# Performance work log

Measured on AMD Instinct MI355X. Metric: run time of the kernel, lower is better.

The kernel has to match this reference:

```python
import jax, jax.numpy as jnp
import numpy as np

B, L, D = 8, 4096, 384
DI, S, DTR, K = 768, 16, 24, 4  # d_inner, d_state, dt_rank, d_conv
NC = 40
EPS = 1e-5


def setup_inputs() -> dict:
    key = jax.random.key(0)
    ks = jax.random.split(key, 12)
    w = 0.02
    return {
        "x": jax.random.normal(ks[0], (B, L, D), jnp.float32),
        "ln_w": jnp.ones((D,), jnp.float32),
        "W_in": jax.random.normal(ks[1], (D, 2 * DI), jnp.float32) * w,
        "conv_w": jax.random.normal(ks[2], (DI, K), jnp.float32) * 0.1,
        "conv_b": jnp.zeros((DI,), jnp.float32),
        "W_xproj": jax.random.normal(ks[3], (DI, DTR + 2 * S), jnp.float32) * w,
        "W_dt": jax.random.normal(ks[4], (DTR, DI), jnp.float32) * 0.1,
        "dt_bias": jnp.full((DI,), -3.0, jnp.float32) + 0.1 * jax.random.normal(ks[5], (DI,), jnp.float32),
        "A_log": jnp.log(1.0 + jax.random.uniform(ks[6], (DI, S), jnp.float32) * 15.0),
        "Dskip": jnp.ones((DI,), jnp.float32),
        "W_out": jax.random.normal(ks[7], (DI, D), jnp.float32) * w,
        "W_fc": jax.random.normal(ks[8], (D, 256), jnp.float32) * w,
        "b_fc": jnp.zeros((256,), jnp.float32),
        "bn_gamma": jnp.ones((256,), jnp.float32),
        "bn_beta": jnp.zeros((256,), jnp.float32),
        "W_cls": jax.random.normal(ks[9], (256, NC), jnp.float32) * w,
        "b_cls": jnp.zeros((NC,), jnp.float32),
    }


def _silu(v):
    return v * jax.nn.sigmoid(v)


def _mamba_block(x, ln_w, W_in, conv_w, conv_b, W_xproj, W_dt, dt_bias, A_log, Dskip, W_out):
    # RMSNorm
    xn = x * jax.lax.rsqrt(jnp.mean(x * x, axis=-1, keepdims=True) + EPS) * ln_w
    xz = xn @ W_in                              # [B,L,2*DI]
    xp, z = jnp.split(xz, 2, axis=-1)
    # causal depthwise conv over sequence
    xp_t = jnp.transpose(xp, (0, 2, 1))         # [B,DI,L]
    xc = jax.lax.conv_general_dilated(
        xp_t, conv_w[:, None, :], window_strides=(1,), padding=[(K - 1, 0)],
        feature_group_count=DI, dimension_numbers=("NCH", "OIH", "NCH"))
    xc = _silu(xc + conv_b[None, :, None])
    xc = jnp.transpose(xc, (0, 2, 1))           # [B,L,DI]
    x_dbl = xc @ W_xproj                        # [B,L,DTR+2S]
    dt_r, Bm, Cm = jnp.split(x_dbl, [DTR, DTR + S], axis=-1)
    dt = jax.nn.softplus(dt_r @ W_dt + dt_bias)  # [B,L,DI]
    A = -jnp.exp(A_log)                          # [DI,S]

    def step(h, t):
        dt_t, B_t, C_t, x_t = t                  # [B,DI],[B,S],[B,S],[B,DI]
        dA = jnp.exp(dt_t[..., None] * A)        # [B,DI,S]
        h = dA * h + (dt_t * x_t)[..., None] * B_t[:, None, :]
        y = jnp.einsum("bds,bs->bd", h, C_t)
        return h, y

    tm = lambda a: jnp.transpose(a, (1, 0, 2))   # time-major
    h0 = jnp.zeros((x.shape[0], DI, S), x.dtype)
    _, ys = jax.lax.scan(step, h0, (tm(dt), tm(Bm), tm(Cm), tm(xc)))
    y = jnp.transpose(ys, (1, 0, 2)) + xc * Dskip  # [B,L,DI]
    y = y * _silu(z)
    return x + y @ W_out                          # residual


def reference(x, ln_w, W_in, conv_w, conv_b, W_xproj, W_dt, dt_bias, A_log,
              Dskip, W_out, W_fc, b_fc, bn_gamma, bn_beta, W_cls, b_cls):
    feats = _mamba_block(x, ln_w, W_in, conv_w, conv_b, W_xproj, W_dt, dt_bias,
                         A_log, Dskip, W_out)
    pooled = jnp.mean(feats, axis=1)             # global pool -> [B,D]
    h = pooled @ W_fc + b_fc                     # Fc
    mu = jnp.mean(h, axis=0)                     # Bn (batch stats)
    var = jnp.var(h, axis=0)
    h = (h - mu) * jax.lax.rsqrt(var + EPS) * bn_gamma + bn_beta
    h = jax.nn.relu(h)                           # Relu (dropout=eval no-op)
    return h @ W_cls + b_cls                     # logits [B,NC]
```

## Files before the change

### kernel.cpp

```cpp
#include <hip/hip_runtime.h>

typedef unsigned short ushort_t;
typedef unsigned int u32;
typedef float f32x4 __attribute__((ext_vector_type(4)));
typedef float f32x2 __attribute__((ext_vector_type(2)));
typedef __bf16 bf16x8 __attribute__((ext_vector_type(8)));

#define B_ 8
#define L_ 4096
#define D_ 384
#define DI_ 768
#define S_ 16
#define NC_ 40
#define ML_ (B_*L_)
#define NCHUNK 32
#define CL 128

constexpr size_t au(size_t x){ return (x + 255) & ~size_t(255); }
constexpr size_t O_FLAG = 0;
constexpr size_t O_LNW  = 256;
constexpr size_t O_CONVW= au(O_LNW  + 384*4);
constexpr size_t O_CONVB= au(O_CONVW+ 3072*4);
constexpr size_t O_WDT  = au(O_CONVB+ 768*4);
constexpr size_t O_DTB  = au(O_WDT  + 18432*4);
constexpr size_t O_A    = au(O_DTB  + 768*4);
constexpr size_t O_DSKIP= au(O_A    + 12288*4);
constexpr size_t O_WOUT = au(O_DSKIP+ 768*4);
constexpr size_t O_WFC  = au(O_WOUT + 294912*4);
constexpr size_t O_BFC  = au(O_WFC  + 98304*4);
constexpr size_t O_GAM  = au(O_BFC  + 256*4);
constexpr size_t O_BET  = au(O_GAM  + 256*4);
constexpr size_t O_WCLS = au(O_BET  + 256*4);
constexpr size_t O_BCLS = au(O_WCLS + 10240*4);
constexpr size_t O_XMEAN= au(O_BCLS + 40*4);
constexpr size_t O_YMEAN= au(O_XMEAN+ 3072*4);
constexpr size_t O_H    = au(O_YMEAN+ 6144*4);
constexpr size_t O_WINT = au(O_H    + 2048*4);
constexpr size_t O_WXT  = au(O_WINT + (size_t)589824*2);
constexpr size_t O_XP   = au(O_WXT  + (size_t)49152*2);
constexpr size_t O_XDBL = O_XP;
constexpr size_t O_FX   = au(O_XDBL + (size_t)ML_*56*4);
constexpr size_t FX_SZ  = (size_t)B_*NCHUNK*49*768*4;
constexpr size_t O_Z    = au(O_XP   + (size_t)ML_*768*2);
constexpr size_t O_XCU  = au(O_Z    + (size_t)ML_*768*2);
constexpr size_t O_XN   = O_XCU;
constexpr size_t O_XC   = O_XCU;
constexpr size_t WS_NEED= O_XCU + (size_t)ML_*768*2;
static_assert(O_FX + FX_SZ <= O_Z, "FX must fit in dead XP tail");

__device__ inline float bf2f(ushort_t u){ return __uint_as_float(((u32)u) << 16); }
__device__ inline ushort_t f2bf(float f){
    u32 x = __float_as_uint(f);
    u32 r = (x + 0x7fffu + ((x >> 16) & 1u)) >> 16;
    return (ushort_t)r;
}
__device__ inline float ldf(const void* p, long i, int flag){
    return flag ? bf2f(((const ushort_t*)p)[i]) : ((const float*)p)[i];
}
__device__ inline ushort_t ldbf(const void* p, long i, int flag){
    return flag ? ((const ushort_t*)p)[i] : f2bf(((const float*)p)[i]);
}
__device__ inline float sigm(float v){ return 1.f / (1.f + __expf(-v)); }

__device__ inline void gload_lds16(const void* g, void* l){
    __builtin_amdgcn_global_load_lds(
        (const __attribute__((address_space(1))) u32*)g,
        (__attribute__((address_space(3))) u32*)l, 16, 0, 0);
}

struct Ptrs { const void* p[17]; };

__global__ void k_detect(const void* x, char* ws){
    __shared__ float s[256];
    int tid = threadIdx.x;
    s[tid] = fabsf(bf2f(((const ushort_t*)x)[tid]));
    __syncthreads();
    for (int st = 128; st > 0; st >>= 1){
        if (tid < st) s[tid] = fmaxf(s[tid], s[tid + st]);
        __syncthreads();
    }
    if (tid == 0) *(int*)(ws + O_FLAG) = (s[0] < 1e4f) ? 1 : 0;
}

#define N_PREP 1082792L
__global__ __launch_bounds__(256) void k_prep(Ptrs ps, char* ws){
    const int flag = *(const int*)(ws + O_FLAG);
    long o = (long)blockIdx.x * 256 + threadIdx.x;
    if (o < 384){ ((float*)(ws+O_LNW))[o]  = ldf(ps.p[1],o,flag); return; }  o -= 384;
    if (o < 3072){ ((float*)(ws+O_CONVW))[o]= ldf(ps.p[3],o,flag); return; } o -= 3072;
    if (o < 768){ ((float*)(ws+O_CONVB))[o]= ldf(ps.p[4],o,flag); return; }  o -= 768;
    if (o < 18432){ ((float*)(ws+O_WDT))[o]= ldf(ps.p[6],o,flag); return; }  o -= 18432;
    if (o < 768){ ((float*)(ws+O_DTB))[o]  = ldf(ps.p[7],o,flag); return; }  o -= 768;
    if (o < 768){ ((float*)(ws+O_DSKIP))[o]= ldf(ps.p[9],o,flag); return; }  o -= 768;
    if (o < 294912){ ((float*)(ws+O_WOUT))[o]= ldf(ps.p[10],o,flag); return; } o -= 294912;
    if (o < 98304){ ((float*)(ws+O_WFC))[o]= ldf(ps.p[11],o,flag); return; } o -= 98304;
    if (o < 256){ ((float*)(ws+O_BFC))[o]  = ldf(ps.p[12],o,flag); return; } o -= 256;
    if (o < 256){ ((float*)(ws+O_GAM))[o]  = ldf(ps.p[13],o,flag); return; } o -= 256;
    if (o < 256){ ((float*)(ws+O_BET))[o]  = ldf(ps.p[14],o,flag); return; } o -= 256;
    if (o < 10240){ ((float*)(ws+O_WCLS))[o]= ldf(ps.p[15],o,flag); return; } o -= 10240;
    if (o < 40){ ((float*)(ws+O_BCLS))[o]  = ldf(ps.p[16],o,flag); return; } o -= 40;
    if (o < 12288){ ((float*)(ws+O_A))[o]  = -__expf(ldf(ps.p[8],o,flag)) * 1.4426950408889634f; return; } o -= 12288;
    if (o < 589824){
        long n = o / 384, k = o % 384;
        ((ushort_t*)(ws+O_WINT))[o] = ldbf(ps.p[2], k*1536 + n, flag); return;
    } o -= 589824;
    if (o < 49152){
        long n = o / 768, k = o % 768;
        ((ushort_t*)(ws+O_WXT))[o] = (n < 56) ? ldbf(ps.p[5], k*56 + n, flag) : (ushort_t)0;
        return;
    } o -= 49152;
    if (o < 3072){ ((float*)(ws+O_XMEAN))[o] = 0.f; return; }
}

__global__ __launch_bounds__(128) void k_rmsnorm(const void* x, char* ws){
    const int flag = *(const int*)(ws + O_FLAG);
    const float* lnw = (const float*)(ws + O_LNW);
    ushort_t* xn = (ushort_t*)(ws + O_XN);
    long row = blockIdx.x;
    int tid = threadIdx.x;
    float v[3];
    if (flag){
        const ushort_t* xb = (const ushort_t*)x;
        #pragma unroll
        for (int c = 0; c < 3; c++) v[c] = bf2f(xb[row*384 + tid + c*128]);
    } else {
        const float* xf = (const float*)x;
        #pragma unroll
        for (int c = 0; c < 3; c++) v[c] = xf[row*384 + tid + c*128];
    }
    __shared__ float red[128];
    red[tid] = v[0]*v[0] + v[1]*v[1] + v[2]*v[2];
    __syncthreads();
    for (int st = 64; st > 0; st >>= 1){
        if (tid < st) red[tid] += red[tid + st];
        __syncthreads();
    }
    float scale = rsqrtf(red[0] * (1.f/384.f) + 1e-5f);
    #pragma unroll
    for (int c = 0; c < 3; c++)
        xn[row*384 + tid + c*128] = f2bf(v[c] * scale * lnw[tid + c*128]);
}

__global__ __launch_bounds__(256) void k_xmean(const void* x, char* ws){
    const int flag = *(const int*)(ws + O_FLAG);
    float* xmean = (float*)(ws + O_XMEAN);
    int b = blockIdx.x, d0 = blockIdx.y*128, l0 = blockIdx.z*256;
    int tid = threadIdx.x, dl = tid & 127, lh = tid >> 7;
    float acc = 0.f;
    if (flag){
        const ushort_t* xb = (const ushort_t*)x;
        for (int l = l0 + lh; l < l0 + 256; l += 2)
            acc += bf2f(xb[((long)b*L_ + l)*384 + d0 + dl]);
    } else {
        const float* xf = (const float*)x;
        for (int l = l0 + lh; l < l0 + 256; l += 2)
            acc += xf[((long)b*L_ + l)*384 + d0 + dl];
    }
    __shared__ float s[256];
    s[tid] = acc; __syncthreads();
    if (tid < 128)
        atomicAdd(&xmean[b*384 + d0 + dl], (s[tid] + s[tid+128]) * (1.f/L_));
}

__global__ __launch_bounds__(256) void k_gemm1(char* ws){
    const ushort_t* xn = (const ushort_t*)(ws + O_XN);
    const ushort_t* wT = (const ushort_t*)(ws + O_WINT);
    ushort_t* xp = (ushort_t*)(ws + O_XP);
    ushort_t* zz = (ushort_t*)(ws + O_Z);
    __shared__ ushort_t sA[128*32];
    __shared__ ushort_t sB[128*32];
    int tid = threadIdx.x, w = tid >> 6, l = tid & 63;
    long m0 = (long)blockIdx.x * 128;
    int n0 = blockIdx.y * 128;
    f32x4 acc[4][4] = {};
    int lr = l >> 2, lk = (l & 3) * 8;
    const ushort_t* gA = xn + (m0 + w*16 + lr)*384 + lk;
    const ushort_t* gB = wT + ((long)(n0 + w*16 + lr))*384 + lk;
    ushort_t* lA = &sA[w*16*32];
    ushort_t* lB = &sB[w*16*32];
    int wm = w & 1, wn = w >> 1;
    int arow = wm*64 + (l & 15);
    int brow = wn*64 + (l & 15);
    int koff = (l >> 4) * 8;
    for (int kc = 0; kc < 12; kc++){
        int k0 = kc * 32;
        gload_lds16(gA + k0,           lA);
        gload_lds16(gA + k0 + 64*384,  lA + 64*32);
        gload_lds16(gB + k0,           lB);
        gload_lds16(gB + k0 + 64*384,  lB + 64*32);
        __syncthreads();
        bf16x8 af[4], bfv[4];
        #pragma unroll
        for (int i = 0; i < 4; i++){
            af[i]  = *(const bf16x8*)&sA[(arow + i*16)*32 + koff];
            bfv[i] = *(const bf16x8*)&sB[(brow + i*16)*32 + koff];
        }
        #pragma unroll
        for (int mb = 0; mb < 4; mb++)
            #pragma unroll
            for (int nb = 0; nb < 4; nb++)
                acc[mb][nb] = __builtin_amdgcn_mfma_f32_16x16x32_bf16(af[mb], bfv[nb], acc[mb][nb], 0, 0, 0);
        __syncthreads();
    }
    ushort_t* outp; int nc0; bool isz;
    if (n0 < 768){ outp = xp; nc0 = n0; isz = false; }
    else { outp = zz; nc0 = n0 - 768; isz = true; }
    int rbase = (l >> 4) * 4, cl = l & 15;
    #pragma unroll
    for (int mb = 0; mb < 4; mb++)
        #pragma unroll
        for (int nb = 0; nb < 4; nb++){
            long row = m0 + wm*64 + mb*16 + rbase;
            int col = nc0 + wn*64 + nb*16 + cl;
            #pragma unroll
            for (int r = 0; r < 4; r++){
                float v = acc[mb][nb][r];
                if (isz) v = v * sigm(v);
                outp[(row + r)*768 + col] = f2bf(v);
            }
        }
}

__global__ __launch_bounds__(256) void k_conv(char* ws){
    const ushort_t* xp = (const ushort_t*)(ws + O_XP);
    ushort_t* xc = (ushort_t*)(ws + O_XC);
    const float* cw = (const float*)(ws + O_CONVW);
    const float* cb = (const float*)(ws + O_CONVB);
    int d = blockIdx.x*256 + threadIdx.x;
    int t0 = blockIdx.y * 8;
    int b = blockIdx.z;
    long rbase = (long)b * L_;
    float w0 = cw[d*4], w1 = cw[d*4+1], w2 = cw[d*4+2], w3 = cw[d*4+3];
    float bias = cb[d];
    float xv[11];
    #pragma unroll
    for (int i = 0; i < 11; i++){
        int t = t0 - 3 + i;
        xv[i] = (t >= 0) ? bf2f(xp[(rbase + t)*768 + d]) : 0.f;
    }
    #pragma unroll
    for (int tt = 0; tt < 8; tt++){
        float v = bias + xv[tt]*w0 + xv[tt+1]*w1 + xv[tt+2]*w2 + xv[tt+3]*w3;
        v = v * sigm(v);
        xc[(rbase + t0 + tt)*768 + d] = f2bf(v);
    }
}

__global__ __launch_bounds__(256) void k_xproj(char* ws){
    const ushort_t* xc = (const ushort_t*)(ws + O_XC);
    const ushort_t* wT = (const ushort_t*)(ws + O_WXT);
    float* xdbl = (float*)(ws + O_XDBL);
    __shared__ ushort_t sA[128*32];
    __shared__ ushort_t sB[64*32];
    int tid = threadIdx.x, w = tid >> 6, l = tid & 63;
    long m0 = (long)blockIdx.x * 128;
    f32x4 acc[2][4] = {};
    int lr = l >> 2, lk = (l & 3) * 8;
    const ushort_t* gA = xc + (m0 + w*16 + lr)*768 + lk;
    const ushort_t* gB = wT + ((long)(w*16 + lr))*768 + lk;
    ushort_t* lA = &sA[w*16*32];
    ushort_t* lB = &sB[w*16*32];
    int arow0 = w*32 + (l & 15);
    int brow = l & 15;
    int koff = (l >> 4) * 8;
    for (int kc = 0; kc < 24; kc++){
        int k0 = kc * 32;
        gload_lds16(gA + k0,           lA);
        gload_lds16(gA + k0 + 64*768,  lA + 64*32);
        gload_lds16(gB + k0,           lB);
        __syncthreads();
        bf16x8 af[2], bfv[4];
        af[0] = *(const bf16x8*)&sA[arow0*32 + koff];
        af[1] = *(const bf16x8*)&sA[(arow0+16)*32 + koff];
        #pragma unroll
        for (int nb = 0; nb < 4; nb++)
            bfv[nb] = *(const bf16x8*)&sB[(nb*16 + brow)*32 + koff];
        #pragma unroll
        for (int mb = 0; mb < 2; mb++)
            #pragma unroll
            for (int nb = 0; nb < 4; nb++)
                acc[mb][nb] = __builtin_amdgcn_mfma_f32_16x16x32_bf16(af[mb], bfv[nb], acc[mb][nb], 0, 0, 0);
        __syncthreads();
    }
    int rbase = (l >> 4) * 4, cl = l & 15;
    #pragma unroll
    for (int mb = 0; mb < 2; mb++)
        #pragma unroll
        for (int nb = 0; nb < 4; nb++){
            int col = nb*16 + cl;
            if (col < 56){
                long row = m0 + w*32 + mb*16 + rbase;
                #pragma unroll
                for (int r = 0; r < 4; r++)
                    xdbl[(row + r)*56 + col] = acc[mb][nb][r];
            }
        }
}

__global__ __launch_bounds__(256, 5) void k_scan(char* ws){
    const ushort_t* xc = (const ushort_t*)(ws + O_XC);
    const ushort_t* wz = (const ushort_t*)(ws + O_Z);
    const float* xdbl = (const float*)(ws + O_XDBL);
    const float* Ag = (const float*)(ws + O_A);
    const float* Dsk = (const float*)(ws + O_DSKIP);
    const float* Wdt = (const float*)(ws + O_WDT);
    const float* dtb = (const float*)(ws + O_DTB);
    float* FX = (float*)(ws + O_FX);
    int tid = threadIdx.x;
    int half = tid & 1, p = tid >> 1;
    int d = blockIdx.x * 128 + p;
    int c = blockIdx.y, b = blockIdx.z;
    long row0 = (long)b * L_ + (long)c * CL;

    __shared__ float sXD[CL*56];
    {
        const f32x4* src = (const f32x4*)(xdbl + row0*56);
        f32x4* dst = (f32x4*)sXD;
        #pragma unroll
        for (int i = 0; i < 7; i++) dst[tid + i*256] = src[tid + i*256];
    }

    f32x2 wdt2[6];
    #pragma unroll
    for (int k = 0; k < 6; k++){
        wdt2[k][0] = Wdt[(half*12 + 2*k    )*768 + d];
        wdt2[k][1] = Wdt[(half*12 + 2*k + 1)*768 + d];
    }
    float dbias = half ? 0.f : dtb[d];
    f32x2 Av2[4];
    #pragma unroll
    for (int j = 0; j < 4; j++){
        Av2[j][0] = Ag[d*16 + half*8 + 2*j];
        Av2[j][1] = Ag[d*16 + half*8 + 2*j + 1];
    }
    float Dv = Dsk[d];
    __syncthreads();

    f32x2 h2[4], q2[4], G2[4];
    #pragma unroll
    for (int j = 0; j < 4; j++){
        h2[j] = f32x2{0.f, 0.f}; G2[j] = f32x2{0.f, 0.f}; q2[j] = f32x2{1.f, 1.f};
    }
    f32x2 ysum2 = {0.f, 0.f};
    float sdw = 0.f;

    const ushort_t* gx = (half ? wz : xc) + row0*768 + d;
    #pragma unroll 8
    for (int t = 0; t < CL; t++){
        ushort_t mine = gx[t*768];
        const float* xd = &sXD[t*56];
        f32x2 acc2 = {dbias, 0.f};
        #pragma unroll
        for (int j = 0; j < 3; j++){
            f32x4 v = *(const f32x4*)&xd[half*12 + j*4];
            acc2 += f32x2{v[0], v[1]} * wdt2[2*j];
            acc2 += f32x2{v[2], v[3]} * wdt2[2*j + 1];
        }
        float dt_p = acc2[0] + acc2[1];
        float dtv = dt_p + __shfl_xor(dt_p, 1);
        float e = __builtin_amdgcn_exp2f(dtv * 1.4426950408889634f);
        float sp = 0.69314718055994531f * __builtin_amdgcn_logf(1.f + e);
        dtv = (dtv > 20.f) ? dtv : sp;

        u32 other = (u32)__shfl_xor((int)(u32)mine, 1);
        float xcv = bf2f(half ? (ushort_t)other : mine);
        float wzv = bf2f(half ? mine : (ushort_t)other);
        float u = dtv * xcv;
        f32x2 u2 = {u, u}, wz2 = {wzv, wzv}, dtv2 = {dtv, dtv};
        f32x4 Bva = *(const f32x4*)&xd[24 + half*8];
        f32x4 Bvb = *(const f32x4*)&xd[28 + half*8];
        f32x4 Cva = *(const f32x4*)&xd[40 + half*8];
        f32x4 Cvb = *(const f32x4*)&xd[44 + half*8];
        #pragma unroll
        for (int j = 0; j < 4; j++){
            f32x2 Bj = (j < 2) ? f32x2{Bva[2*j], Bva[2*j+1]} : f32x2{Bvb[2*j-4], Bvb[2*j-3]};
            f32x2 Cj = (j < 2) ? f32x2{Cva[2*j], Cva[2*j+1]} : f32x2{Cvb[2*j-4], Cvb[2*j-3]};
            f32x2 arg = dtv2 * Av2[j];
            f32x2 dA;
            dA[0] = __builtin_amdgcn_exp2f(arg[0]);
            dA[1] = __builtin_amdgcn_exp2f(arg[1]);
            h2[j] = dA * h2[j] + u2 * Bj;
            f32x2 Cw = Cj * wz2;
            ysum2 += h2[j] * Cw;
            q2[j] = q2[j] * dA;
            G2[j] += q2[j] * Cw;
        }
        sdw += xcv * wzv;
    }
    float ys = ysum2[0] + ysum2[1] + (half ? 0.f : Dv * sdw);
    ys += __shfl_xor(ys, 1);
    long fb = ((long)(b*NCHUNK + c)*49)*768 + d;
    if (!half) FX[fb] = ys;
    #pragma unroll
    for (int j = 0; j < 4; j++){
        int sg = half*8 + 2*j;
        FX[fb + (1+sg)*768]  = h2[j][0];  FX[fb + (2+sg)*768]  = h2[j][1];
        FX[fb + (17+sg)*768] = q2[j][0];  FX[fb + (18+sg)*768] = q2[j][1];
        FX[fb + (33+sg)*768] = G2[j][0];  FX[fb + (34+sg)*768] = G2[j][1];
    }
}

__global__ __launch_bounds__(256) void k_fix(char* ws){
    const float* FX = (const float*)(ws + O_FX);
    float* ymean = (float*)(ws + O_YMEAN);
    int tid = threadIdx.x;
    int dl = tid & 15, s = tid >> 4;
    int d = blockIdx.x * 16 + dl;
    int b = blockIdx.y;
    float Hrun = 0.f, ys = 0.f;
    for (int c = 0; c < NCHUNK; c++){
        long fb = ((long)(b*NCHUNK + c)*49)*768 + d;
        float Gs = FX[fb + (33+s)*768];
        float Hs = FX[fb + (1+s)*768];
        float qs = FX[fb + (17+s)*768];
        ys += Hrun * Gs;
        if (s == 0) ys += FX[fb];
        Hrun = Hs + qs * Hrun;
    }
    __shared__ float sR[256];
    sR[tid] = ys;
    __syncthreads();
    #pragma unroll
    for (int st = 8; st >= 1; st >>= 1){
        if (s < st) sR[tid] += sR[tid + st*16];
        __syncthreads();
    }
    if (s == 0) ymean[b*768 + d] = sR[dl] * (1.f/L_);
}

__global__ __launch_bounds__(256) void k_head1(char* ws){
    const float* ymean = (const float*)(ws + O_YMEAN);
    const float* xmean = (const float*)(ws + O_XMEAN);
    const float* Wout = (const float*)(ws + O_WOUT);
    const float* Wfc = (const float*)(ws + O_WFC);
    const float* bfc = (const float*)(ws + O_BFC);
    float* hbuf = (float*)(ws + O_H);
    int b = blockIdx.x, tid = threadIdx.x;
    __shared__ float sY[768];
    __shared__ float sP[384];
    sY[tid] = ymean[b*768 + tid];
    sY[tid+256] = ymean[b*768 + tid + 256];
    sY[tid+512] = ymean[b*768 + tid + 512];
    __syncthreads();
    for (int d = tid; d < 384; d += 256){
        float v = xmean[b*384 + d];
        for (int i = 0; i < 768; i++) v += sY[i] * Wout[i*384 + d];
        sP[d] = v;
    }
    __syncthreads();
    float v = bfc[tid];
    for (int dd = 0; dd < 384; dd++) v += sP[dd] * Wfc[dd*256 + tid];
    hbuf[b*256 + tid] = v;
}

__global__ __launch_bounds__(384) void k_head2(char* ws, void* out){
    const int flag = *(const int*)(ws + O_FLAG);
    const float* hbuf = (const float*)(ws + O_H);
    const float* gam = (const float*)(ws + O_GAM);
    const float* bet = (const float*)(ws + O_BET);
    const float* Wcls = (const float*)(ws + O_WCLS);
    const float* bcls = (const float*)(ws + O_BCLS);
    int tid = threadIdx.x;
    __shared__ float sH[8*256];
    if (tid < 256){
        float hv[8]; float mu = 0.f;
        #pragma unroll
        for (int b = 0; b < 8; b++){ hv[b] = hbuf[b*256 + tid]; mu += hv[b]; }
        mu *= 0.125f;
        float var = 0.f;
        #pragma unroll
        for (int b = 0; b < 8; b++){ float dv = hv[b]-mu; var += dv*dv; }
        var *= 0.125f;
        float rs = rsqrtf(var + 1e-5f);
        #pragma unroll
        for (int b = 0; b < 8; b++){
            float t = (hv[b]-mu)*rs*gam[tid] + bet[tid];
            sH[b*256 + tid] = t > 0.f ? t : 0.f;
        }
    }
    __syncthreads();
    if (tid < 320){
        int b = tid / 40, c = tid % 40;
        float acc = bcls[c];
        for (int j = 0; j < 256; j++) acc += sH[b*256 + j] * Wcls[j*40 + c];
        if (flag) ((ushort_t*)out)[b*40 + c] = f2bf(acc);
        else      ((float*)out)[b*40 + c] = acc;
    }
}

extern "C" void kernel_launch(void* const* d_in, const int* in_sizes, int n_in,
                              void* d_out, int out_size, void* d_ws, size_t ws_size,
                              hipStream_t stream){
    (void)in_sizes; (void)n_in; (void)out_size; (void)ws_size;
    char* ws = (char*)d_ws;
    Ptrs ps;
    for (int i = 0; i < 17; i++) ps.p[i] = d_in[i];

    k_detect<<<1, 256, 0, stream>>>(d_in[0], ws);
    k_prep<<<(unsigned)((N_PREP + 255) / 256), 256, 0, stream>>>(ps, ws);
    k_rmsnorm<<<ML_, 128, 0, stream>>>(d_in[0], ws);
    k_xmean<<<dim3(8, 3, 16), 256, 0, stream>>>(d_in[0], ws);
    k_gemm1<<<dim3(ML_/128, 12), 256, 0, stream>>>(ws);
    k_conv<<<dim3(3, L_/8, B_), 256, 0, stream>>>(ws);
    k_xproj<<<ML_/128, 256, 0, stream>>>(ws);
    k_scan<<<dim3(6, NCHUNK, B_), 256, 0, stream>>>(ws);
    k_fix<<<dim3(48, B_), 256, 0, stream>>>(ws);
    k_head1<<<B_, 256, 0, stream>>>(ws);
    k_head2<<<1, 384, 0, stream>>>(ws, d_out);
}
```

Baseline: 509.3 us.

## Use wave-per-row RMSNorm, halve scan shared memory, restructure chunk fix

RMSNorm now processes four rows per block with one wavefront per row, reducing with shuffles instead of a shared-memory tree with barriers. The scan kernel stages its per-chunk xdbl slice in two halves of 64 timesteps, halving shared memory, and raises the launch-bounds occupancy hint from 5 to 8. The fix kernel gives each thread four state indices and 64 channels per block, which shortens the reduction. The tighter occupancy hint may force register spills in the scan, and the extra barrier between halves adds a small stall.

Measured after the change: 1.068 ms. 2.1x slower.

```diff
diff --git a/kernel.cpp b/kernel.cpp
--- a/kernel.cpp
+++ b/kernel.cpp
@@ -112,33 +112,32 @@
     if (o < 3072){ ((float*)(ws+O_XMEAN))[o] = 0.f; return; }
 }
 
-__global__ __launch_bounds__(128) void k_rmsnorm(const void* x, char* ws){
+__global__ __launch_bounds__(256) void k_rmsnorm(const void* x, char* ws){
     const int flag = *(const int*)(ws + O_FLAG);
     const float* lnw = (const float*)(ws + O_LNW);
     ushort_t* xn = (ushort_t*)(ws + O_XN);
-    long row = blockIdx.x;
     int tid = threadIdx.x;
-    float v[3];
+    int lane = tid & 63;
+    long row = (long)blockIdx.x * 4 + (tid >> 6);
+    float v[6];
     if (flag){
-        const ushort_t* xb = (const ushort_t*)x;
-        #pragma unroll
-        for (int c = 0; c < 3; c++) v[c] = bf2f(xb[row*384 + tid + c*128]);
+        const ushort_t* xb = (const ushort_t*)x + row*384;
+        #pragma unroll
+        for (int c = 0; c < 6; c++) v[c] = bf2f(xb[lane + c*64]);
     } else {
-        const float* xf = (const float*)x;
-        #pragma unroll
-        for (int c = 0; c < 3; c++) v[c] = xf[row*384 + tid + c*128];
-    }
-    __shared__ float red[128];
-    red[tid] = v[0]*v[0] + v[1]*v[1] + v[2]*v[2];
-    __syncthreads();
-    for (int st = 64; st > 0; st >>= 1){
-        if (tid < st) red[tid] += red[tid + st];
-        __syncthreads();
-    }
-    float scale = rsqrtf(red[0] * (1.f/384.f) + 1e-5f);
-    #pragma unroll
-    for (int c = 0; c < 3; c++)
-        xn[row*384 + tid + c*128] = f2bf(v[c] * scale * lnw[tid + c*128]);
+        const float* xf = (const float*)x + row*384;
+        #pragma unroll
+        for (int c = 0; c < 6; c++) v[c] = xf[lane + c*64];
+    }
+    float ss = 0.f;
+    #pragma unroll
+    for (int c = 0; c < 6; c++) ss += v[c]*v[c];
+    #pragma unroll
+    for (int st = 1; st < 64; st <<= 1) ss += __shfl_xor(ss, st);
+    float scale = rsqrtf(ss * (1.f/384.f) + 1e-5f);
+    #pragma unroll
+    for (int c = 0; c < 6; c++)
+        xn[row*384 + lane + c*64] = f2bf(v[c] * scale * lnw[lane + c*64]);
 }
 
 __global__ __launch_bounds__(256) void k_xmean(const void* x, char* ws){
@@ -297,7 +296,7 @@
         }
 }
 
-__global__ __launch_bounds__(256, 5) void k_scan(char* ws){
+__global__ __launch_bounds__(256, 8) void k_scan(char* ws){
     const ushort_t* xc = (const ushort_t*)(ws + O_XC);
     const ushort_t* wz = (const ushort_t*)(ws + O_Z);
     const float* xdbl = (const float*)(ws + O_XDBL);
@@ -312,13 +311,7 @@
     int c = blockIdx.y, b = blockIdx.z;
     long row0 = (long)b * L_ + (long)c * CL;
 
-    __shared__ float sXD[CL*56];
-    {
-        const f32x4* src = (const f32x4*)(xdbl + row0*56);
-        f32x4* dst = (f32x4*)sXD;
-        #pragma unroll
-        for (int i = 0; i < 7; i++) dst[tid + i*256] = src[tid + i*256];
-    }
+    __shared__ float sXD[64*56];
 
     f32x2 wdt2[6];
     #pragma unroll
@@ -334,7 +327,6 @@
         Av2[j][1] = Ag[d*16 + half*8 + 2*j + 1];
     }
     float Dv = Dsk[d];
-    __syncthreads();
 
     f32x2 h2[4], q2[4], G2[4];
     #pragma unroll
@@ -345,47 +337,59 @@
     float sdw = 0.f;
 
     const ushort_t* gx = (half ? wz : xc) + row0*768 + d;
-    #pragma unroll 8
-    for (int t = 0; t < CL; t++){
-        ushort_t mine = gx[t*768];
-        const float* xd = &sXD[t*56];
-        f32x2 acc2 = {dbias, 0.f};
-        #pragma unroll
-        for (int j = 0; j < 3; j++){
-            f32x4 v = *(const f32x4*)&xd[half*12 + j*4];
-            acc2 += f32x2{v[0], v[1]} * wdt2[2*j];
-            acc2 += f32x2{v[2], v[3]} * wdt2[2*j + 1];
-        }
-        float dt_p = acc2[0] + acc2[1];
-        float dtv = dt_p + __shfl_xor(dt_p, 1);
-        float e = __builtin_amdgcn_exp2f(dtv * 1.4426950408889634f);
-        float sp = 0.69314718055994531f * __builtin_amdgcn_logf(1.f + e);
-        dtv = (dtv > 20.f) ? dtv : sp;
-
-        u32 other = (u32)__shfl_xor((int)(u32)mine, 1);
-        float xcv = bf2f(half ? (ushort_t)other : mine);
-        float wzv = bf2f(half ? mine : (ushort_t)other);
-        float u = dtv * xcv;
-        f32x2 u2 = {u, u}, wz2 = {wzv, wzv}, dtv2 = {dtv, dtv};
-        f32x4 Bva = *(const f32x4*)&xd[24 + half*8];
-        f32x4 Bvb = *(const f32x4*)&xd[28 + half*8];
-        f32x4 Cva = *(const f32x4*)&xd[40 + half*8];
-        f32x4 Cvb = *(const f32x4*)&xd[44 + half*8];
-        #pragma unroll
-        for (int j = 0; j < 4; j++){
-            f32x2 Bj = (j < 2) ? f32x2{Bva[2*j], Bva[2*j+1]} : f32x2{Bvb[2*j-4], Bvb[2*j-3]};
-            f32x2 Cj = (j < 2) ? f32x2{Cva[2*j], Cva[2*j+1]} : f32x2{Cvb[2*j-4], Cvb[2*j-3]};
-            f32x2 arg = dtv2 * Av2[j];
-            f32x2 dA;
-            dA[0] = __builtin_amdgcn_exp2f(arg[0]);
-            dA[1] = __builtin_amdgcn_exp2f(arg[1]);
-            h2[j] = dA * h2[j] + u2 * Bj;
-            f32x2 Cw = Cj * wz2;
-            ysum2 += h2[j] * Cw;
-            q2[j] = q2[j] * dA;
-            G2[j] += q2[j] * Cw;
-        }
-        sdw += xcv * wzv;
+
+    for (int hh = 0; hh < 2; hh++){
+        __syncthreads();
+        {
+            const f32x2* src = (const f32x2*)(xdbl + (row0 + hh*64)*56);
+            f32x2* dst = (f32x2*)sXD;
+            #pragma unroll
+            for (int i = 0; i < 7; i++) dst[tid + i*256] = src[tid + i*256];
+        }
+        __syncthreads();
+        #pragma unroll 8
+        for (int tt = 0; tt < 64; tt++){
+            int t = hh*64 + tt;
+            ushort_t mine = gx[t*768];
+            const float* xd = &sXD[tt*56];
+            f32x2 acc2 = {dbias, 0.f};
+            #pragma unroll
+            for (int j = 0; j < 3; j++){
+                f32x4 v = *(const f32x4*)&xd[half*12 + j*4];
+                acc2 += f32x2{v[0], v[1]} * wdt2[2*j];
+                acc2 += f32x2{v[2], v[3]} * wdt2[2*j + 1];
+            }
+            float dt_p = acc2[0] + acc2[1];
+            float dtv = dt_p + __shfl_xor(dt_p, 1);
+            float e = __builtin_amdgcn_exp2f(dtv * 1.4426950408889634f);
+            float sp = 0.69314718055994531f * __builtin_amdgcn_logf(1.f + e);
+            dtv = (dtv > 20.f) ? dtv : sp;
+
+            u32 other = (u32)__shfl_xor((int)(u32)mine, 1);
+            float xcv = bf2f(half ? (ushort_t)other : mine);
+            float wzv = bf2f(half ? mine : (ushort_t)other);
+            float u = dtv * xcv;
+            f32x2 u2 = {u, u}, wz2 = {wzv, wzv}, dtv2 = {dtv, dtv};
+            f32x4 Bva = *(const f32x4*)&xd[24 + half*8];
+            f32x4 Bvb = *(const f32x4*)&xd[28 + half*8];
+            f32x4 Cva = *(const f32x4*)&xd[40 + half*8];
+            f32x4 Cvb = *(const f32x4*)&xd[44 + half*8];
+            #pragma unroll
+            for (int j = 0; j < 4; j++){
+                f32x2 Bj = (j < 2) ? f32x2{Bva[2*j], Bva[2*j+1]} : f32x2{Bvb[2*j-4], Bvb[2*j-3]};
+                f32x2 Cj = (j < 2) ? f32x2{Cva[2*j], Cva[2*j+1]} : f32x2{Cvb[2*j-4], Cvb[2*j-3]};
+                f32x2 arg = dtv2 * Av2[j];
+                f32x2 dA;
+                dA[0] = __builtin_amdgcn_exp2f(arg[0]);
+                dA[1] = __builtin_amdgcn_exp2f(arg[1]);
+                h2[j] = dA * h2[j] + u2 * Bj;
+                f32x2 Cw = Cj * wz2;
+                ysum2 += h2[j] * Cw;
+                q2[j] = q2[j] * dA;
+                G2[j] += q2[j] * Cw;
+            }
+            sdw += xcv * wzv;
+        }
     }
     float ys = ysum2[0] + ysum2[1] + (half ? 0.f : Dv * sdw);
     ys += __shfl_xor(ys, 1);
@@ -404,28 +408,30 @@
     const float* FX = (const float*)(ws + O_FX);
     float* ymean = (float*)(ws + O_YMEAN);
     int tid = threadIdx.x;
-    int dl = tid & 15, s = tid >> 4;
-    int d = blockIdx.x * 16 + dl;
+    int dl = tid & 63, sg = tid >> 6;
+    int d = blockIdx.x * 64 + dl;
     int b = blockIdx.y;
-    float Hrun = 0.f, ys = 0.f;
+    float Hrun[4] = {0.f, 0.f, 0.f, 0.f};
+    float ys = 0.f;
     for (int c = 0; c < NCHUNK; c++){
         long fb = ((long)(b*NCHUNK + c)*49)*768 + d;
-        float Gs = FX[fb + (33+s)*768];
-        float Hs = FX[fb + (1+s)*768];
-        float qs = FX[fb + (17+s)*768];
-        ys += Hrun * Gs;
-        if (s == 0) ys += FX[fb];
-        Hrun = Hs + qs * Hrun;
+        if (sg == 0) ys += FX[fb];
+        #pragma unroll
+        for (int k = 0; k < 4; k++){
+            int s = sg*4 + k;
+            float Gs = FX[fb + (33+s)*768];
+            float Hs = FX[fb + (1+s)*768];
+            float qs = FX[fb + (17+s)*768];
+            ys += Hrun[k] * Gs;
+            Hrun[k] = Hs + qs * Hrun[k];
+        }
     }
     __shared__ float sR[256];
     sR[tid] = ys;
     __syncthreads();
-    #pragma unroll
-    for (int st = 8; st >= 1; st >>= 1){
-        if (s < st) sR[tid] += sR[tid + st*16];
-        __syncthreads();
-    }
-    if (s == 0) ymean[b*768 + d] = sR[dl] * (1.f/L_);
+    if (sg < 2) sR[tid] += sR[tid + 128];
+    __syncthreads();
+    if (sg == 0) ymean[b*768 + d] = (sR[dl] + sR[dl + 64]) * (1.f/L_);
 }
 
 __global__ __launch_bounds__(256) void k_head1(char* ws){
@@ -498,13 +504,13 @@
 
     k_detect<<<1, 256, 0, stream>>>(d_in[0], ws);
     k_prep<<<(unsigned)((N_PREP + 255) / 256), 256, 0, stream>>>(ps, ws);
-    k_rmsnorm<<<ML_, 128, 0, stream>>>(d_in[0], ws);
+    k_rmsnorm<<<ML_/4, 256, 0, stream>>>(d_in[0], ws);
     k_xmean<<<dim3(8, 3, 16), 256, 0, stream>>>(d_in[0], ws);
     k_gemm1<<<dim3(ML_/128, 12), 256, 0, stream>>>(ws);
     k_conv<<<dim3(3, L_/8, B_), 256, 0, stream>>>(ws);
     k_xproj<<<ML_/128, 256, 0, stream>>>(ws);
     k_scan<<<dim3(6, NCHUNK, B_), 256, 0, stream>>>(ws);
-    k_fix<<<dim3(48, B_), 256, 0, stream>>>(ws);
+    k_fix<<<dim3(12, B_), 256, 0, stream>>>(ws);
     k_head1<<<B_, 256, 0, stream>>>(ws);
     k_head2<<<1, 384, 0, stream>>>(ws, d_out);
 }
```
